# Performance work log

Measured on AMD Instinct MI355X. Metric: run time of the kernel, lower is better.

Reference implementation:

```python
import jax, jax.numpy as jnp
import numpy as np
import math

K = 1.0          # Lorentz manifold curvature param: points satisfy <x,x>_L = -K
NUM_HEADS = 16
EPS = 1e-6
B, L, D = 2, 2048, 1024


def lorentz_inner(x, y):
    # <x,y>_L = -x0*y0 + sum_{i>0} xi*yi  (over last dim)
    return jnp.sum(x * y, axis=-1) - 2.0 * x[..., 0] * y[..., 0]


def project_to_lorentz(z):
    # treat z[...,1:] as space components, recompute time so <x,x>_L = -K
    space = z[..., 1:]
    time = jnp.sqrt(K + jnp.sum(space * space, axis=-1, keepdims=True))
    return jnp.concatenate([time, space], axis=-1)


def hlinear(x, W, b, num_heads):
    # Lorentz linear layer (Chen et al. 2022): Euclidean affine map on the
    # ambient coordinates followed by curvature-aware time re-normalization.
    z = x @ W.T + b  # (B, L, D)
    if num_heads > 0:
        Bz, Lz, Dz = z.shape
        z = z.reshape(Bz, Lz, num_heads, Dz // num_heads)  # (B, L, H, dh)
    return project_to_lorentz(z)


def setup_inputs() -> dict:
    key = jax.random.key(0)
    ks = jax.random.split(key, 8)
    def mk_point(k):
        # random manifold points: random space part, valid time coordinate
        z = jax.random.normal(k, (B, L, D), dtype=jnp.float32) * 0.5
        return project_to_lorentz(z)
    scale = 1.0 / math.sqrt(D)
    def mk_w(k):
        return jax.random.normal(k, (D, D), dtype=jnp.float32) * scale
    return {
        "query": mk_point(ks[0]),
        "key": mk_point(ks[1]),
        "value": mk_point(ks[2]),
        "W_Q": mk_w(ks[3]), "b_Q": jnp.zeros((D,), jnp.float32),
        "W_K": mk_w(ks[4]), "b_K": jnp.zeros((D,), jnp.float32),
        "W_V": mk_w(ks[5]), "b_V": jnp.zeros((D,), jnp.float32),
        "W_O": mk_w(ks[6]), "b_O": jnp.zeros((D,), jnp.float32),
    }


def reference(query, key, value, W_Q, b_Q, W_K, b_K, W_V, b_V, W_O, b_O):
    H = NUM_HEADS
    q = hlinear(query, W_Q, b_Q, H)  # (B, L, H, dh) on per-head Lorentz manifold
    k = hlinear(key, W_K, b_K, H)
    v = hlinear(value, W_V, b_V, H)
    dh = q.shape[-1]
    # Lorentzian inner products <q_i, k_j>_L per head: (B, H, Lq, Lk)
    ip = (jnp.einsum('bqhd,bkhd->bhqk', q, k)
          - 2.0 * jnp.einsum('bqh,bkh->bhqk', q[..., 0], k[..., 0]))
    # negative squared Lorentz distance: -d_L^2 = 2K + 2<q,k>_L, scaled by sqrt(dh)
    scores = (2.0 * K + 2.0 * ip) * (1.0 / math.sqrt(dh))
    attn = jax.nn.softmax(scores, axis=-1)
    # Lorentzian centroid aggregation (Law et al.): normalize weighted sum back
    # onto the hyperboloid.
    mu = jnp.einsum('bhqk,bkhd->bqhd', attn, v)  # (B, L, H, dh)
    norm = jnp.sqrt(jnp.maximum(jnp.abs(lorentz_inner(mu, mu)), EPS))
    out_heads = math.sqrt(K) * mu / norm[..., None]
    cat = out_heads.reshape(out_heads.shape[0], out_heads.shape[1], -1)  # (B, L, D)
    return hlinear(cat, W_O, b_O, 0)  # (B, L, D) on the manifold
```

## Files before the change

### kernel.cpp

```cpp
#include <hip/hip_runtime.h>
#include <math.h>

namespace {
constexpr int Ln = 2048;
constexpr int Dn = 1024;
constexpr int Mn = 4096;
constexpr float QSCALE = 0.25f * 1.44269504088896340736f;
}

typedef unsigned short u16;
typedef unsigned int u32;
typedef __attribute__((ext_vector_type(4))) float f32x4;
typedef __attribute__((ext_vector_type(8))) __bf16 bf16x8;
typedef __attribute__((ext_vector_type(4))) unsigned short u16x4;
typedef __attribute__((ext_vector_type(8))) unsigned short u16x8;
typedef __attribute__((ext_vector_type(4))) unsigned int u32x4;


__device__ __forceinline__ u16 f2bf(float f) {
    union { float f; unsigned u; } cv; cv.f = f;
    unsigned u = cv.u + 0x7fffu + ((cv.u >> 16) & 1u);
    return (u16)(u >> 16);
}
__device__ __forceinline__ float bf2f(u16 h) {
    union { unsigned u; float f; } cv; cv.u = ((unsigned)h) << 16;
    return cv.f;
}

__device__ __forceinline__ u32 pkbf(float a, float b) {
    union { __bf16 h[2]; u32 u; } cv;
    cv.h[0] = (__bf16)a; cv.h[1] = (__bf16)b;
    return cv.u;
}

#if __has_builtin(__builtin_amdgcn_exp2f)
__device__ __forceinline__ float exp2_fast(float x) {
    return __builtin_amdgcn_exp2f(x);
}
#else
__device__ __forceinline__ float exp2_fast(float x) {
    float r;
    asm("v_exp_f32 %0, %1" : "=v"(r) : "v"(x));
    return r;
}
#endif

template <int CTRL>
__device__ __forceinline__ float dppf(float x) {
    return __int_as_float(__builtin_amdgcn_update_dpp(
        0, __float_as_int(x), CTRL, 0xf, 0xf, true));
}
__device__ __forceinline__ float red16_add(float x) {
    x += dppf<0xB1>(x);
    x += dppf<0x4E>(x);
    x += dppf<0x141>(x);
    x += dppf<0x140>(x);
    return x;
}

__device__ __forceinline__ void gload16(const void* g, void* l) {
    __builtin_amdgcn_global_load_lds(
        (const __attribute__((address_space(1))) unsigned int*)g,
        (__attribute__((address_space(3))) unsigned int*)l, 16, 0, 0);
}

__global__ __launch_bounds__(256)
void cvt_in3(const float* __restrict__ i0, const float* __restrict__ i1,
             const float* __restrict__ i2,
             u16* __restrict__ o0, u16* __restrict__ o1, u16* __restrict__ o2)
{
    const int z = blockIdx.y;
    const float* in = z == 0 ? i0 : (z == 1 ? i1 : i2);
    u16* out       = z == 0 ? o0 : (z == 1 ? o1 : o2);
    int i = blockIdx.x * 256 + threadIdx.x;
    f32x4 v = ((const f32x4*)in)[i];
    u16x4 o;
#pragma unroll
    for (int j = 0; j < 4; ++j) o[j] = f2bf(v[j]);
    int l = i >> 8;
    int e = (i & 255) * 4;
    int idx = l * 1024 + (e & ~63) + (((((e >> 3) & 7) ^ (l & 7))) << 3) + (e & 7);
    *(u16x4*)&out[idx] = o;
}

__global__ __launch_bounds__(256)
void cvt_w(const float* __restrict__ w0, const float* __restrict__ w1,
           const float* __restrict__ w2, const float* __restrict__ w3,
           u16* __restrict__ q0, u16* __restrict__ q1,
           u16* __restrict__ q2, u16* __restrict__ q3)
{
    const int z = blockIdx.y;
    int i = blockIdx.x * 256 + threadIdx.x;
    if (z < 3) {
        const float* in = z == 0 ? w0 : (z == 1 ? w1 : w2);
        u16* out       = z == 0 ? q0 : (z == 1 ? q1 : q2);
        f32x4 v = ((const f32x4*)in)[i];
        u16x4 o;
#pragma unroll
        for (int j = 0; j < 4; ++j) o[j] = f2bf(v[j]);
        int l = i >> 8;
        int e = (i & 255) * 4;
        int idx = l * 1024 + (e & ~63) + (((((e >> 3) & 7) ^ (l & 7))) << 3) + (e & 7);
        *(u16x4*)&out[idx] = o;
    } else {
        int o  = i >> 8;
        int s0 = (i & 255) * 4;
        int h = s0 >> 6, sl = s0 & 63, a = sl >> 2;
        const float* src = w3 + (size_t)o * 1024 + h * 64;
        u16x4 ov = { f2bf(src[a]), f2bf(src[16 + a]),
                     f2bf(src[32 + a]), f2bf(src[48 + a]) };
        int idx = o * 1024 + h * 64 + (((sl >> 3) ^ (o & 7)) << 3) + (sl & 7);
        *(u16x4*)&q3[idx] = ov;
    }
}

__device__ __forceinline__
void gemm_proj_body(const u16* __restrict__ A, const u16* __restrict__ W,
                    const float* __restrict__ bias, u16* __restrict__ Ct,
                    float scale, float tsign, u16* As, u16* Bs)
{
    const int t = threadIdx.x;
    const int lane = t & 63, w = t >> 6;
    const int g = lane >> 4, c = lane & 15;
    const int wr = w >> 1, wc = w & 1;
    const int bm = blockIdx.y * 128, bn = blockIdx.x * 128;

    f32x4 acc[4][4];
    const f32x4 z4 = {0.f, 0.f, 0.f, 0.f};
#pragma unroll
    for (int i = 0; i < 4; ++i)
#pragma unroll
        for (int j = 0; j < 4; ++j) acc[i][j] = z4;

    for (int k0 = 0; k0 < Dn; k0 += 64) {
        __syncthreads();
#pragma unroll
        for (int p = 0; p < 4; ++p) {
            int ci = p * 256 + t;
            int r = ci >> 3, bq = ci & 7;
            gload16(A + (size_t)(bm + r) * Dn + k0 + bq * 8, &As[ci * 8]);
            gload16(W + (size_t)(bn + r) * Dn + k0 + bq * 8, &Bs[ci * 8]);
        }
        __syncthreads();
#pragma unroll
        for (int kk = 0; kk < 2; ++kk) {
            bf16x8 a[4], b[4];
#pragma unroll
            for (int mi = 0; mi < 4; ++mi)
                a[mi] = *(const bf16x8*)&As[(wr * 64 + mi * 16 + c) * 64 +
                                            (((kk * 4 + g) ^ (c & 7)) << 3)];
#pragma unroll
            for (int ni = 0; ni < 4; ++ni)
                b[ni] = *(const bf16x8*)&Bs[(wc * 64 + ni * 16 + c) * 64 +
                                            (((kk * 4 + g) ^ (c & 7)) << 3)];
            __builtin_amdgcn_s_setprio(1);
#pragma unroll
            for (int mi = 0; mi < 4; ++mi)
#pragma unroll
                for (int ni = 0; ni < 4; ++ni)
                    acc[mi][ni] = __builtin_amdgcn_mfma_f32_16x16x32_bf16(
                        a[mi], b[ni], acc[mi][ni], 0, 0, 0);
            __builtin_amdgcn_s_setprio(0);
        }
    }

    const int hcb = bn + wc * 64;
    const int h = hcb >> 6;
#pragma unroll
    for (int mi = 0; mi < 4; ++mi)
#pragma unroll
        for (int j = 0; j < 4; ++j) {
            int ll = bm + wr * 64 + mi * 16 + g * 4 + j;
            float zv[4];
#pragma unroll
            for (int ni = 0; ni < 4; ++ni)
                zv[ni] = acc[mi][ni][j] + bias[hcb + ni * 16 + c];
            float loc = zv[0]*zv[0] + zv[1]*zv[1] + zv[2]*zv[2] + zv[3]*zv[3];
            if (c == 0) loc -= zv[0] * zv[0];
            loc = red16_add(loc);
            float tval = sqrtf(1.f + loc);
            float v0 = (c == 0) ? tsign * tval : zv[0];
            int bb = ll >> 11, l2 = ll & 2047;
            u16* dst = Ct + (((size_t)bb * 16 + h) * Ln + l2) * 64;
            u16x4 pkv = { f2bf(v0 * scale), f2bf(zv[1] * scale),
                          f2bf(zv[2] * scale), f2bf(zv[3] * scale) };
            *(u16x4*)&dst[(4 * c) ^ ((ll & 7) << 3)] = pkv;
        }
}

__global__ __launch_bounds__(256)
void gemm_qkv(const u16* __restrict__ xq, const u16* __restrict__ xk,
              const u16* __restrict__ xv, const u16* __restrict__ wq,
              const u16* __restrict__ wk, const u16* __restrict__ wv,
              const float* __restrict__ bq, const float* __restrict__ bk,
              const float* __restrict__ bv,
              u16* __restrict__ oq, u16* __restrict__ ok, u16* __restrict__ ov)
{
    __shared__ u16 As[128 * 64];
    __shared__ u16 Bs[128 * 64];
    const int z = blockIdx.z;
    const u16* A = z == 0 ? xq : (z == 1 ? xk : xv);
    const u16* W = z == 0 ? wq : (z == 1 ? wk : wv);
    const float* bb = z == 0 ? bq : (z == 1 ? bk : bv);
    u16* O = z == 0 ? oq : (z == 1 ? ok : ov);
    gemm_proj_body(A, W, bb, O, z == 0 ? QSCALE : 1.f, z == 0 ? -1.f : 1.f, As, Bs);
}

__global__ __launch_bounds__(256)
void transpose_v(const u16* __restrict__ vin, u16* __restrict__ vout)
{
    __shared__ u16 raw[64 * 64];
    const int t = threadIdx.x;
    const int bh = blockIdx.x, lc = blockIdx.y;
    const u16* src = vin + ((size_t)bh * Ln + lc * 64) * 64;
#pragma unroll
    for (int p = 0; p < 2; ++p) {
        int ci = p * 256 + t;
        *(u16x8*)&raw[ci * 8] = *(const u16x8*)(src + ci * 8);
    }
    __syncthreads();
    const int d = t >> 2, cp0 = (t & 3) * 16;
    const int s = ((d & 15) << 2) | (d >> 4);
    u16 buf[16];
#pragma unroll
    for (int i = 0; i < 16; ++i) {
        int cp = cp0 + i;
        int n = ((cp >> 5) << 5) | (((cp >> 2) & 1) << 4) | (((cp >> 3) & 3) << 2) | (cp & 3);
        buf[i] = raw[n * 64 + ((((s >> 3) ^ (n & 7)) << 3) | (s & 7))];
    }
    u16* dst = vout + ((size_t)bh * 64 + d) * Ln + lc * 64;
    int b0 = cp0 >> 3;
    *(u16x8*)&dst[((b0 ^ (d & 7)) << 3)]       = *(const u16x8*)&buf[0];
    *(u16x8*)&dst[(((b0 + 1) ^ (d & 7)) << 3)] = *(const u16x8*)&buf[8];
}

__global__ __launch_bounds__(256, 4)
void attn_mfma(const u16* __restrict__ qt, const u16* __restrict__ kt,
               const u16* __restrict__ vT, u16* __restrict__ part)
{
    __shared__ u16 smem[4 * 4096];

    const int t = threadIdx.x;
    const int lane = t & 63, w = t >> 6;
    const int g = lane >> 4, c = lane & 15;
    const int id  = blockIdx.x;
    const int qb  = (id >> 3) & 15;
    const int gidx = (id & 7) | ((id >> 7) << 3);
    const int bh  = gidx & 31;
    const int kvh = gidx >> 5;
    const int q0  = qb * 128;
    const u16* Q = qt + (size_t)bh * Ln * 64;
    const u16* K = kt + (size_t)bh * Ln * 64 + (size_t)kvh * (1024 * 64);
    const u16* V = vT + (size_t)bh * 64 * (size_t)Ln + kvh * 1024;

    bf16x8 qa[2][2];
#pragma unroll
    for (int mi = 0; mi < 2; ++mi)
#pragma unroll
        for (int kk = 0; kk < 2; ++kk) {
            int row = q0 + w * 32 + mi * 16 + c;
            qa[mi][kk] = *(const bf16x8*)(Q + (size_t)row * 64 +
                                          (((kk * 4 + g) ^ (c & 7)) << 3));
        }

    f32x4 o[2][4];
    const f32x4 z4 = {0.f, 0.f, 0.f, 0.f};
#pragma unroll
    for (int mi = 0; mi < 2; ++mi)
#pragma unroll
        for (int di = 0; di < 4; ++di) o[mi][di] = z4;

    const int fb0 = c * 128 + (((0 + g) ^ (c & 7)) << 4);
    const int fb1 = c * 128 + (((4 + g) ^ (c & 7)) << 4);

    char* sb = (char*)smem;
    const int cr = t >> 3, cb = t & 7;
    const u16* kp = K + (size_t)cr * 64 + cb * 8;
    const u16* vp = V + (size_t)cr * Ln + cb * 8;

    gload16(kp,            sb + t * 16);
    gload16(kp + 2048,     sb + 4096 + t * 16);
    gload16(vp,            sb + 16384 + t * 16);
    gload16(vp + 32 * Ln,  sb + 16384 + 4096 + t * 16);

    constexpr int NC = 1024 / 64;
    for (int ch = 0; ch < NC; ++ch) {
        __syncthreads();
        if (ch + 1 < NC) {
            const u16* kn = kp + (ch + 1) * 4096;
            const u16* vn = vp + (ch + 1) * 64;
            char* db = sb + (((ch + 1) & 1) << 13);
            gload16(kn,           db + t * 16);
            gload16(kn + 2048,    db + 4096 + t * 16);
            gload16(vn,           db + 16384 + t * 16);
            gload16(vn + 32 * Ln, db + 16384 + 4096 + t * 16);
        }
        const char* kbb = sb + ((ch & 1) << 13);
        const char* vbb = kbb + 16384;

        f32x4 sf[2][4];
#pragma unroll
        for (int mi = 0; mi < 2; ++mi)
#pragma unroll
            for (int ni = 0; ni < 4; ++ni) sf[mi][ni] = z4;
        __builtin_amdgcn_s_setprio(1);
#pragma unroll
        for (int kk = 0; kk < 2; ++kk) {
            const int fb = kk ? fb1 : fb0;
            bf16x8 kb[4];
#pragma unroll
            for (int ni = 0; ni < 4; ++ni)
                kb[ni] = *(const bf16x8*)(kbb + fb + ni * 2048);
#pragma unroll
            for (int mi = 0; mi < 2; ++mi)
#pragma unroll
                for (int ni = 0; ni < 4; ++ni)
                    sf[mi][ni] = __builtin_amdgcn_mfma_f32_16x16x32_bf16(
                        kb[ni], qa[mi][kk], sf[mi][ni], 0, 0, 0);
        }
        __builtin_amdgcn_s_setprio(0);

        bf16x8 paf[2][2];
#pragma unroll
        for (int mi = 0; mi < 2; ++mi) {
            float ex[4][4];
#pragma unroll
            for (int ni = 0; ni < 4; ++ni)
#pragma unroll
                for (int j = 0; j < 4; ++j)
                    ex[ni][j] = exp2_fast(sf[mi][ni][j]);
            u32x4 p0 = { pkbf(ex[0][0], ex[0][1]), pkbf(ex[0][2], ex[0][3]),
                         pkbf(ex[1][0], ex[1][1]), pkbf(ex[1][2], ex[1][3]) };
            u32x4 p1 = { pkbf(ex[2][0], ex[2][1]), pkbf(ex[2][2], ex[2][3]),
                         pkbf(ex[3][0], ex[3][1]), pkbf(ex[3][2], ex[3][3]) };
            paf[mi][0] = __builtin_bit_cast(bf16x8, p0);
            paf[mi][1] = __builtin_bit_cast(bf16x8, p1);
        }

        __builtin_amdgcn_s_setprio(1);
#pragma unroll
        for (int kk = 0; kk < 2; ++kk) {
            const int fb = kk ? fb1 : fb0;
#pragma unroll
            for (int di = 0; di < 4; ++di) {
                bf16x8 vb = *(const bf16x8*)(vbb + fb + di * 2048);
#pragma unroll
                for (int mi = 0; mi < 2; ++mi)
                    o[mi][di] = __builtin_amdgcn_mfma_f32_16x16x32_bf16(
                        paf[mi][kk], vb, o[mi][di], 0, 0, 0);
            }
        }
        __builtin_amdgcn_s_setprio(0);
    }

    u16* P = part + (size_t)(kvh * 32 + bh) * (4 * 2048 * 16);
#pragma unroll
    for (int mi = 0; mi < 2; ++mi)
#pragma unroll
        for (int j = 0; j < 4; ++j) {
            int row = q0 + w * 32 + mi * 16 + g * 4 + j;
#pragma unroll
            for (int di = 0; di < 4; ++di)
                P[(di * 2048 + row) * 16 + c] = f2bf(o[mi][di][j]);
        }
}

__global__ __launch_bounds__(256)
void attn_combine(const u16* __restrict__ part, u16* __restrict__ cat)
{
    const int grp = blockIdx.x * 16 + (threadIdx.x >> 4);
    const int c = threadIdx.x & 15;
    const int bh = grp >> 11, q = grp & 2047;
    const u16* P0 = part + (size_t)bh * (4 * 2048 * 16);
    const u16* P1 = part + (size_t)(32 + bh) * (4 * 2048 * 16);
    float mu[4];
#pragma unroll
    for (int di = 0; di < 4; ++di) {
        int idx = (di * 2048 + q) * 16 + c;
        mu[di] = bf2f(P0[idx]) + bf2f(P1[idx]);
    }
    float loc = mu[0]*mu[0] + mu[1]*mu[1] + mu[2]*mu[2] + mu[3]*mu[3];
    if (c == 0) loc -= 2.f * mu[0] * mu[0];
    loc = red16_add(loc);
    float rn = rsqrtf(fmaxf(fabsf(loc), 1e-6f));
    const int b = bh >> 4, h = bh & 15;
    u16* dst = cat + ((size_t)b * Ln + q) * Dn + h * 64;
    u16x4 pkv = { f2bf(mu[0] * rn), f2bf(mu[1] * rn),
                  f2bf(mu[2] * rn), f2bf(mu[3] * rn) };
    *(u16x4*)&dst[(4 * c) ^ ((q & 7) << 3)] = pkv;
}

__global__ __launch_bounds__(256)
void gemm_o(const u16* __restrict__ A, const u16* __restrict__ B,
            const float* __restrict__ bias, float* __restrict__ C)
{
    __shared__ u16 As[64 * 64];
    __shared__ u16 Bs[128 * 64];
    const int t = threadIdx.x;
    const int lane = t & 63, w = t >> 6;
    const int g = lane >> 4, c = lane & 15;
    const int wr = w >> 1, wc = w & 1;
    const int bm = blockIdx.y * 64, bn = blockIdx.x * 128;

    f32x4 acc[2][4];
    const f32x4 z4 = {0.f, 0.f, 0.f, 0.f};
#pragma unroll
    for (int i = 0; i < 2; ++i)
#pragma unroll
        for (int j = 0; j < 4; ++j) acc[i][j] = z4;

    for (int k0 = 0; k0 < Dn; k0 += 64) {
        __syncthreads();
#pragma unroll
        for (int p = 0; p < 2; ++p) {
            int ci = p * 256 + t;
            gload16(A + (size_t)(bm + (ci >> 3)) * Dn + k0 + (ci & 7) * 8,
                    &As[ci * 8]);
        }
#pragma unroll
        for (int p = 0; p < 4; ++p) {
            int ci = p * 256 + t;
            gload16(B + (size_t)(bn + (ci >> 3)) * Dn + k0 + (ci & 7) * 8,
                    &Bs[ci * 8]);
        }
        __syncthreads();
#pragma unroll
        for (int kk = 0; kk < 2; ++kk) {
            bf16x8 a[2], b[4];
#pragma unroll
            for (int mi = 0; mi < 2; ++mi)
                a[mi] = *(const bf16x8*)&As[(wr * 32 + mi * 16 + c) * 64 +
                                            (((kk * 4 + g) ^ (c & 7)) << 3)];
#pragma unroll
            for (int ni = 0; ni < 4; ++ni)
                b[ni] = *(const bf16x8*)&Bs[(wc * 64 + ni * 16 + c) * 64 +
                                            (((kk * 4 + g) ^ (c & 7)) << 3)];
            __builtin_amdgcn_s_setprio(1);
#pragma unroll
            for (int mi = 0; mi < 2; ++mi)
#pragma unroll
                for (int ni = 0; ni < 4; ++ni)
                    acc[mi][ni] = __builtin_amdgcn_mfma_f32_16x16x32_bf16(
                        a[mi], b[ni], acc[mi][ni], 0, 0, 0);
            __builtin_amdgcn_s_setprio(0);
        }
    }

#pragma unroll
    for (int mi = 0; mi < 2; ++mi)
#pragma unroll
        for (int j = 0; j < 4; ++j) {
            size_t row = bm + wr * 32 + mi * 16 + g * 4 + j;
#pragma unroll
            for (int ni = 0; ni < 4; ++ni) {
                int col = bn + wc * 64 + ni * 16 + c;
                C[row * Dn + col] = acc[mi][ni][j] + bias[col];
            }
        }
}

__global__ __launch_bounds__(256)
void lorentz_row_full(float* __restrict__ z)
{
    __shared__ float red[4];
    const int t = threadIdx.x;
    const size_t base = (size_t)blockIdx.x * Dn;
    float4 v = *(const float4*)&z[base + t * 4];
    if (t == 0) v.x = 0.f;
    float ssq = v.x * v.x + v.y * v.y + v.z * v.z + v.w * v.w;
#pragma unroll
    for (int off = 32; off; off >>= 1) ssq += __shfl_xor(ssq, off);
    if ((t & 63) == 0) red[t >> 6] = ssq;
    __syncthreads();
    if (t == 0) z[base] = sqrtf(1.0f + red[0] + red[1] + red[2] + red[3]);
}

extern "C" void kernel_launch(void* const* d_in, const int* in_sizes, int n_in,
                              void* d_out, int out_size, void* d_ws, size_t ws_size,
                              hipStream_t stream)
{
    const float* query = (const float*)d_in[0];
    const float* key_  = (const float*)d_in[1];
    const float* value = (const float*)d_in[2];
    const float* W_Q   = (const float*)d_in[3];
    const float* b_Q   = (const float*)d_in[4];
    const float* W_K   = (const float*)d_in[5];
    const float* b_K   = (const float*)d_in[6];
    const float* W_V   = (const float*)d_in[7];
    const float* b_V   = (const float*)d_in[8];
    const float* W_O   = (const float*)d_in[9];
    const float* b_O   = (const float*)d_in[10];

    const size_t MD = (size_t)Mn * Dn;
    const size_t DD = (size_t)Dn * Dn;
    u16* xq   = (u16*)d_ws;
    u16* xk   = xq + MD;
    u16* xv   = xk + MD;
    u16* wo   = xv + MD;
    u16* q_t  = wo + DD;
    u16* k_t  = q_t + MD;
    u16* wq   = k_t + MD;
    u16* wk   = wq + DD;
    u16* wv   = wk + DD;
    u16* v_ln = wv + DD;
    u16* part = wq;
    u16* v_T  = xv;
    u16* cat  = xk;

    dim3 ci(Mn * Dn / 1024, 3);
    cvt_in3<<<ci, 256, 0, stream>>>(query, key_, value, xq, xk, xv);
    dim3 cw(Dn * Dn / 1024, 4);
    cvt_w<<<cw, 256, 0, stream>>>(W_Q, W_K, W_V, W_O, wq, wk, wv, wo);

    dim3 gq(Dn / 128, Mn / 128, 3);
    gemm_qkv<<<gq, 256, 0, stream>>>(xq, xk, xv, wq, wk, wv,
                                     b_Q, b_K, b_V, q_t, k_t, v_ln);

    dim3 tg(32, Ln / 64);
    transpose_v<<<tg, 256, 0, stream>>>(v_ln, v_T);

    attn_mfma<<<1024, 256, 0, stream>>>(q_t, k_t, v_T, part);

    attn_combine<<<4096, 256, 0, stream>>>(part, cat);

    dim3 go(Dn / 128, Mn / 64);
    gemm_o<<<go, 256, 0, stream>>>(cat, wo, b_O, (float*)d_out);
    lorentz_row_full<<<Mn, 256, 0, stream>>>((float*)d_out);
}
```

Before: 140.4 us.

## Double-buffer LDS in projection GEMMs and remap blocks to 1D grouped order

Both the QKV and output projection GEMMs now use two LDS buffers, prefetching the next k-slice while computing the current one, with one barrier per step instead of two. The QKV GEMM tile shrinks from 128x128 to 64x128, doubling the block count and raising occupancy. Blocks use a 1D launch with a grouped mapping of M tiles for better cache reuse of weight tiles. LDS use per block goes up and fewer MFMAs per wave lower arithmetic intensity.

```diff
diff --git a/kernel.cpp b/kernel.cpp
--- a/kernel.cpp
+++ b/kernel.cpp
@@ -114,48 +114,71 @@
     }
 }
 
-__device__ __forceinline__
-void gemm_proj_body(const u16* __restrict__ A, const u16* __restrict__ W,
-                    const float* __restrict__ bias, u16* __restrict__ Ct,
-                    float scale, float tsign, u16* As, u16* Bs)
-{
+__global__ __launch_bounds__(256)
+void gemm_qkv(const u16* __restrict__ xq, const u16* __restrict__ xk,
+              const u16* __restrict__ xv, const u16* __restrict__ wq,
+              const u16* __restrict__ wk, const u16* __restrict__ wv,
+              const float* __restrict__ bq, const float* __restrict__ bk,
+              const float* __restrict__ bv,
+              u16* __restrict__ oq, u16* __restrict__ ok, u16* __restrict__ ov)
+{
+    __shared__ u16 As[2][64 * 64];
+    __shared__ u16 Bs[2][128 * 64];
     const int t = threadIdx.x;
     const int lane = t & 63, w = t >> 6;
     const int g = lane >> 4, c = lane & 15;
     const int wr = w >> 1, wc = w & 1;
-    const int bm = blockIdx.y * 128, bn = blockIdx.x * 128;
-
-    f32x4 acc[4][4];
+    const int id = blockIdx.x;
+    const int bm = ((id & 7) * 8 + ((id >> 3) & 7)) * 64;
+    const int bn = ((id >> 6) & 7) * 128;
+    const int z  = id >> 9;
+
+    const u16* A = z == 0 ? xq : (z == 1 ? xk : xv);
+    const u16* W = z == 0 ? wq : (z == 1 ? wk : wv);
+    const float* bias = z == 0 ? bq : (z == 1 ? bk : bv);
+    u16* Ct = z == 0 ? oq : (z == 1 ? ok : ov);
+    const float scale = z == 0 ? QSCALE : 1.f;
+    const float tsign = z == 0 ? -1.f : 1.f;
+
+    f32x4 acc[2][4];
     const f32x4 z4 = {0.f, 0.f, 0.f, 0.f};
 #pragma unroll
-    for (int i = 0; i < 4; ++i)
+    for (int i = 0; i < 2; ++i)
 #pragma unroll
         for (int j = 0; j < 4; ++j) acc[i][j] = z4;
 
-    for (int k0 = 0; k0 < Dn; k0 += 64) {
+    const int sr = t >> 3, sb2 = (t & 7) * 8;
+    const u16* Ap = A + (size_t)(bm + sr) * Dn + sb2;
+    const u16* Wp = W + (size_t)(bn + sr) * Dn + sb2;
+
+    auto stage = [&](int buf, int k0) {
+        gload16(Ap + k0,            &As[buf][t * 8]);
+        gload16(Ap + 32 * Dn + k0,  &As[buf][(256 + t) * 8]);
+        gload16(Wp + k0,            &Bs[buf][t * 8]);
+        gload16(Wp + 32 * Dn + k0,  &Bs[buf][(256 + t) * 8]);
+        gload16(Wp + 64 * Dn + k0,  &Bs[buf][(512 + t) * 8]);
+        gload16(Wp + 96 * Dn + k0,  &Bs[buf][(768 + t) * 8]);
+    };
+
+    stage(0, 0);
+    for (int ki = 0; ki < 16; ++ki) {
         __syncthreads();
-#pragma unroll
-        for (int p = 0; p < 4; ++p) {
-            int ci = p * 256 + t;
-            int r = ci >> 3, bq = ci & 7;
-            gload16(A + (size_t)(bm + r) * Dn + k0 + bq * 8, &As[ci * 8]);
-            gload16(W + (size_t)(bn + r) * Dn + k0 + bq * 8, &Bs[ci * 8]);
-        }
-        __syncthreads();
+        if (ki + 1 < 16) stage((ki + 1) & 1, (ki + 1) * 64);
+        const u16* as = As[ki & 1];
+        const u16* bs = Bs[ki & 1];
 #pragma unroll
         for (int kk = 0; kk < 2; ++kk) {
-            bf16x8 a[4], b[4];
-#pragma unroll
-            for (int mi = 0; mi < 4; ++mi)
-                a[mi] = *(const bf16x8*)&As[(wr * 64 + mi * 16 + c) * 64 +
-                                            (((kk * 4 + g) ^ (c & 7)) << 3)];
+            const int so = ((kk * 4 + g) ^ (c & 7)) << 3;
+            bf16x8 a[2], b[4];
+#pragma unroll
+            for (int mi = 0; mi < 2; ++mi)
+                a[mi] = *(const bf16x8*)&as[(wr * 32 + mi * 16 + c) * 64 + so];
 #pragma unroll
             for (int ni = 0; ni < 4; ++ni)
-                b[ni] = *(const bf16x8*)&Bs[(wc * 64 + ni * 16 + c) * 64 +
-                                            (((kk * 4 + g) ^ (c & 7)) << 3)];
+                b[ni] = *(const bf16x8*)&bs[(wc * 64 + ni * 16 + c) * 64 + so];
             __builtin_amdgcn_s_setprio(1);
 #pragma unroll
-            for (int mi = 0; mi < 4; ++mi)
+            for (int mi = 0; mi < 2; ++mi)
 #pragma unroll
                 for (int ni = 0; ni < 4; ++ni)
                     acc[mi][ni] = __builtin_amdgcn_mfma_f32_16x16x32_bf16(
@@ -167,10 +190,10 @@
     const int hcb = bn + wc * 64;
     const int h = hcb >> 6;
 #pragma unroll
-    for (int mi = 0; mi < 4; ++mi)
+    for (int mi = 0; mi < 2; ++mi)
 #pragma unroll
         for (int j = 0; j < 4; ++j) {
-            int ll = bm + wr * 64 + mi * 16 + g * 4 + j;
+            int ll = bm + wr * 32 + mi * 16 + g * 4 + j;
             float zv[4];
 #pragma unroll
             for (int ni = 0; ni < 4; ++ni)
@@ -189,24 +212,6 @@
 }
 
 __global__ __launch_bounds__(256)
-void gemm_qkv(const u16* __restrict__ xq, const u16* __restrict__ xk,
-              const u16* __restrict__ xv, const u16* __restrict__ wq,
-              const u16* __restrict__ wk, const u16* __restrict__ wv,
-              const float* __restrict__ bq, const float* __restrict__ bk,
-              const float* __restrict__ bv,
-              u16* __restrict__ oq, u16* __restrict__ ok, u16* __restrict__ ov)
-{
-    __shared__ u16 As[128 * 64];
-    __shared__ u16 Bs[128 * 64];
-    const int z = blockIdx.z;
-    const u16* A = z == 0 ? xq : (z == 1 ? xk : xv);
-    const u16* W = z == 0 ? wq : (z == 1 ? wk : wv);
-    const float* bb = z == 0 ? bq : (z == 1 ? bk : bv);
-    u16* O = z == 0 ? oq : (z == 1 ? ok : ov);
-    gemm_proj_body(A, W, bb, O, z == 0 ? QSCALE : 1.f, z == 0 ? -1.f : 1.f, As, Bs);
-}
-
-__global__ __launch_bounds__(256)
 void transpose_v(const u16* __restrict__ vin, u16* __restrict__ vout)
 {
     __shared__ u16 raw[64 * 64];
@@ -394,13 +399,15 @@
 void gemm_o(const u16* __restrict__ A, const u16* __restrict__ B,
             const float* __restrict__ bias, float* __restrict__ C)
 {
-    __shared__ u16 As[64 * 64];
-    __shared__ u16 Bs[128 * 64];
+    __shared__ u16 As[2][64 * 64];
+    __shared__ u16 Bs[2][128 * 64];
     const int t = threadIdx.x;
     const int lane = t & 63, w = t >> 6;
     const int g = lane >> 4, c = lane & 15;
     const int wr = w >> 1, wc = w & 1;
-    const int bm = blockIdx.y * 64, bn = blockIdx.x * 128;
+    const int id = blockIdx.x;
+    const int bm = ((id & 7) * 8 + ((id >> 3) & 7)) * 64;
+    const int bn = (id >> 6) * 128;
 
     f32x4 acc[2][4];
     const f32x4 z4 = {0.f, 0.f, 0.f, 0.f};
@@ -409,32 +416,35 @@
 #pragma unroll
         for (int j = 0; j < 4; ++j) acc[i][j] = z4;
 
-    for (int k0 = 0; k0 < Dn; k0 += 64) {
+    const int sr = t >> 3, sb2 = (t & 7) * 8;
+    const u16* Ap = A + (size_t)(bm + sr) * Dn + sb2;
+    const u16* Bp = B + (size_t)(bn + sr) * Dn + sb2;
+
+    auto stage = [&](int buf, int k0) {
+        gload16(Ap + k0,            &As[buf][t * 8]);
+        gload16(Ap + 32 * Dn + k0,  &As[buf][(256 + t) * 8]);
+        gload16(Bp + k0,            &Bs[buf][t * 8]);
+        gload16(Bp + 32 * Dn + k0,  &Bs[buf][(256 + t) * 8]);
+        gload16(Bp + 64 * Dn + k0,  &Bs[buf][(512 + t) * 8]);
+        gload16(Bp + 96 * Dn + k0,  &Bs[buf][(768 + t) * 8]);
+    };
+
+    stage(0, 0);
+    for (int ki = 0; ki < 16; ++ki) {
         __syncthreads();
-#pragma unroll
-        for (int p = 0; p < 2; ++p) {
-            int ci = p * 256 + t;
-            gload16(A + (size_t)(bm + (ci >> 3)) * Dn + k0 + (ci & 7) * 8,
-                    &As[ci * 8]);
-        }
-#pragma unroll
-        for (int p = 0; p < 4; ++p) {
-            int ci = p * 256 + t;
-            gload16(B + (size_t)(bn + (ci >> 3)) * Dn + k0 + (ci & 7) * 8,
-                    &Bs[ci * 8]);
-        }
-        __syncthreads();
+        if (ki + 1 < 16) stage((ki + 1) & 1, (ki + 1) * 64);
+        const u16* as = As[ki & 1];
+        const u16* bs = Bs[ki & 1];
 #pragma unroll
         for (int kk = 0; kk < 2; ++kk) {
+            const int so = ((kk * 4 + g) ^ (c & 7)) << 3;
             bf16x8 a[2], b[4];
 #pragma unroll
             for (int mi = 0; mi < 2; ++mi)
-                a[mi] = *(const bf16x8*)&As[(wr * 32 + mi * 16 + c) * 64 +
-                                            (((kk * 4 + g) ^ (c & 7)) << 3)];
+                a[mi] = *(const bf16x8*)&as[(wr * 32 + mi * 16 + c) * 64 + so];
 #pragma unroll
             for (int ni = 0; ni < 4; ++ni)
-                b[ni] = *(const bf16x8*)&Bs[(wc * 64 + ni * 16 + c) * 64 +
-                                            (((kk * 4 + g) ^ (c & 7)) << 3)];
+                b[ni] = *(const bf16x8*)&bs[(wc * 64 + ni * 16 + c) * 64 + so];
             __builtin_amdgcn_s_setprio(1);
 #pragma unroll
             for (int mi = 0; mi < 2; ++mi)
@@ -512,9 +522,8 @@
     dim3 cw(Dn * Dn / 1024, 4);
     cvt_w<<<cw, 256, 0, stream>>>(W_Q, W_K, W_V, W_O, wq, wk, wv, wo);
 
-    dim3 gq(Dn / 128, Mn / 128, 3);
-    gemm_qkv<<<gq, 256, 0, stream>>>(xq, xk, xv, wq, wk, wv,
-                                     b_Q, b_K, b_V, q_t, k_t, v_ln);
+    gemm_qkv<<<1536, 256, 0, stream>>>(xq, xk, xv, wq, wk, wv,
+                                       b_Q, b_K, b_V, q_t, k_t, v_ln);
 
     dim3 tg(32, Ln / 64);
     transpose_v<<<tg, 256, 0, stream>>>(v_ln, v_T);
@@ -523,7 +532,6 @@
 
     attn_combine<<<4096, 256, 0, stream>>>(part, cat);
 
-    dim3 go(Dn / 128, Mn / 64);
-    gemm_o<<<go, 256, 0, stream>>>(cat, wo, b_O, (float*)d_out);
+    gemm_o<<<512, 256, 0, stream>>>(cat, wo, b_O, (float*)d_out);
     lorentz_row_full<<<Mn, 256, 0, stream>>>((float*)d_out);
 }
```

New measurement: 124.3 us, median of 2. 1.13x faster.
